# Performance work log

Hardware: AMD Instinct MI355X
Metric: run time of the kernel (lower is better)

The kernel has to match this reference:

```python
import jax, jax.numpy as jnp
import numpy as np

H = 8
D = 512
DK = D // H
B = 16
N = 8192


def setup_inputs() -> dict:
    key = jax.random.key(0)
    k1, k2, k3, k4 = jax.random.split(key, 4)
    x = jax.random.normal(k1, (B, N, D), dtype=jnp.float32)
    W_k = jax.random.normal(k2, (D, D), dtype=jnp.float32) * (1.0 / np.sqrt(D))
    W_g = jax.random.normal(k3, (D, D), dtype=jnp.float32) * (1.0 / np.sqrt(D))
    query = jax.random.normal(k4, (H, 1, DK), dtype=jnp.float32)
    return {"x": x, "W_k": W_k, "W_g": W_g, "query": query}


def reference(x, W_k, W_g, query):
    b, n, d = x.shape
    # nn.Linear: y = x @ W.T  (no bias)
    K = (x @ W_k.T).reshape(b, n, H, DK).transpose(0, 2, 1, 3)  # (b,h,n,dk)
    G = (x @ W_g.T).reshape(b, n, H, DK).transpose(0, 2, 1, 3)  # (b,h,n,dk)
    xh = x.reshape(b, n, H, DK).transpose(0, 2, 1, 3)           # (b,h,n,dk)
    gated = jnp.tanh(K) * jax.nn.sigmoid(G)                     # (b,h,n,dk)
    # single-query attention: scores (b,h,1,n)
    scores = jnp.einsum('hmd,bhnd->bhmn', query, gated)
    attn = jax.nn.softmax(scores, axis=-1)
    out = jnp.einsum('bhmn,bhnd->bhmd', attn, xh)               # (b,h,1,dk)
    out = out.transpose(0, 2, 1, 3).reshape(b, 1, H * DK)
    return out.squeeze()  # (b, d)
```

## Files before the change

kernel.cpp:

```cpp
#include <hip/hip_runtime.h>
#include <hip/hip_bf16.h>

#define H_ 8
#define D_ 512
#define DK_ 64
#define B_ 16
#define N_ 8192
#define M_ (B_ * N_)

typedef __attribute__((ext_vector_type(8))) short short8;
typedef __attribute__((ext_vector_type(4))) float floatx4;

__device__ __forceinline__ void glds16(const void* g, void* l) {
    __builtin_amdgcn_global_load_lds((const __attribute__((address_space(1))) void*)g,
                                     (__attribute__((address_space(3))) void*)l,
                                     16, 0, 0);
}

__device__ __forceinline__ unsigned short f2bf(float f) {
    unsigned u = __float_as_uint(f);
    return (unsigned short)((u + 0x7fffu + ((u >> 16) & 1u)) >> 16);
}

__device__ __forceinline__ unsigned pack_bf2(float x, float y) {
    return __builtin_amdgcn_perm(__float_as_uint(y) + 0x8000u,
                                 __float_as_uint(x) + 0x8000u, 0x07060302u);
}

__global__ __launch_bounds__(256) void cvt_kernel(const float* __restrict__ src,
                                                  unsigned short* __restrict__ dst, int n4) {
    int i = blockIdx.x * blockDim.x + threadIdx.x;
    int stride = gridDim.x * blockDim.x;
    for (; i < n4; i += stride) {
        float4 v = ((const float4*)src)[i];
        ushort4 o;
        o.x = f2bf(v.x); o.y = f2bf(v.y); o.z = f2bf(v.z); o.w = f2bf(v.w);
        ((ushort4*)dst)[i] = o;
    }
}

__global__ __launch_bounds__(256, 2) void gemm_score_kernel(
    const float* __restrict__ x,
    const unsigned short* __restrict__ wkb,
    const unsigned short* __restrict__ wgb,
    const float* __restrict__ query,
    float* __restrict__ s_buf)
{
    __shared__ float lds_a[128 * 32];
    __shared__ unsigned short lds_k[128 * 32];
    __shared__ unsigned short lds_g[128 * 32];

    const int t = threadIdx.x;
    const int lane = t & 63;
    const int wave = t >> 6;
    const int wm = wave >> 1, wn = wave & 1;
    const int jc = blockIdx.x * 128;
    const int m0 = blockIdx.y * 128;

    floatx4 acc_k[4][4], acc_g[4][4];
#pragma unroll
    for (int i = 0; i < 4; ++i)
#pragma unroll
        for (int j = 0; j < 4; ++j) { acc_k[i][j] = (floatx4)0.f; acc_g[i][j] = (floatx4)0.f; }

    int ar[4], ac[4];
#pragma unroll
    for (int i = 0; i < 4; ++i) {
        int p = i * 256 + t;
        int r = p >> 3;
        ar[i] = r;
        ac[i] = (p & 7) ^ (r & 7);
    }
    int br[2], bc[2];
#pragma unroll
    for (int i = 0; i < 2; ++i) {
        int p = i * 256 + t;
        int r = p >> 2;
        br[i] = r;
        bc[i] = (p & 3) ^ ((r >> 1) & 3);
    }

    const int fr = lane & 15;
    const int q  = lane >> 4;
    const int sw_a0 = (2 * q) ^ (fr & 7);
    const int sw_a1 = sw_a0 ^ 1;
    const int sw_b  = q ^ ((fr >> 1) & 3);

    for (int k0 = 0; k0 < 512; k0 += 32) {
#pragma unroll
        for (int i = 0; i < 4; ++i)
            glds16(x + (size_t)(m0 + ar[i]) * 512 + k0 + ac[i] * 4,
                   lds_a + (size_t)(i * 256 + t) * 4);
#pragma unroll
        for (int i = 0; i < 2; ++i) {
            glds16(wkb + (size_t)(jc + br[i]) * 512 + k0 + bc[i] * 8,
                   lds_k + (size_t)(i * 256 + t) * 8);
            glds16(wgb + (size_t)(jc + br[i]) * 512 + k0 + bc[i] * 8,
                   lds_g + (size_t)(i * 256 + t) * 8);
        }
        __syncthreads();

        short8 a[4], bk[4], bg[4];
#pragma unroll
        for (int mi = 0; mi < 4; ++mi) {
            int r = wm * 64 + mi * 16 + fr;
            float4 f0 = *(const float4*)(lds_a + (r * 8 + sw_a0) * 4);
            float4 f1 = *(const float4*)(lds_a + (r * 8 + sw_a1) * 4);
            union { unsigned u[4]; short8 s; } tmp;
            tmp.u[0] = pack_bf2(f0.x, f0.y);
            tmp.u[1] = pack_bf2(f0.z, f0.w);
            tmp.u[2] = pack_bf2(f1.x, f1.y);
            tmp.u[3] = pack_bf2(f1.z, f1.w);
            a[mi] = tmp.s;
        }
#pragma unroll
        for (int ni = 0; ni < 4; ++ni) {
            int r = wn * 64 + ni * 16 + fr;
            bk[ni] = *(const short8*)(lds_k + (r * 4 + sw_b) * 8);
            bg[ni] = *(const short8*)(lds_g + (r * 4 + sw_b) * 8);
        }
#pragma unroll
        for (int mi = 0; mi < 4; ++mi)
#pragma unroll
            for (int ni = 0; ni < 4; ++ni) {
                acc_k[mi][ni] = __builtin_amdgcn_mfma_f32_16x16x32_bf16(a[mi], bk[ni], acc_k[mi][ni], 0, 0, 0);
                acc_g[mi][ni] = __builtin_amdgcn_mfma_f32_16x16x32_bf16(a[mi], bg[ni], acc_g[mi][ni], 0, 0, 0);
            }
        __syncthreads();
    }

    const int h = blockIdx.x * 2 + wn;
    float qv[4];
#pragma unroll
    for (int ni = 0; ni < 4; ++ni) qv[ni] = query[h * 64 + ni * 16 + fr];

#pragma unroll
    for (int mi = 0; mi < 4; ++mi) {
#pragma unroll
        for (int r = 0; r < 4; ++r) {
            float v = 0.f;
#pragma unroll
            for (int ni = 0; ni < 4; ++ni) {
                float kv = acc_k[mi][ni][r];
                float gv = acc_g[mi][ni][r];
                float e2k = __expf(2.f * kv);
                float th = 1.f - 2.f / (e2k + 1.f);
                float sg = 1.f / (1.f + __expf(-gv));
                v += qv[ni] * th * sg;
            }
            v += __shfl_xor(v, 1);
            v += __shfl_xor(v, 2);
            v += __shfl_xor(v, 4);
            v += __shfl_xor(v, 8);
            if (fr == 0) {
                int mg = m0 + wm * 64 + mi * 16 + (lane >> 4) * 4 + r;
                int b = mg >> 13, n = mg & 8191;
                s_buf[((size_t)(b * 8 + h) << 13) + n] = v;
            }
        }
    }
}

__global__ __launch_bounds__(256) void stats_kernel(const float* __restrict__ s_buf,
                                                    float* __restrict__ mb, float* __restrict__ lb) {
    const int bh = blockIdx.x;
    const float* s = s_buf + ((size_t)bh << 13);
    const int t = threadIdx.x;
    float mx = -3.0e38f;
    for (int i = t; i < 8192; i += 256) mx = fmaxf(mx, s[i]);
#pragma unroll
    for (int m = 32; m > 0; m >>= 1) mx = fmaxf(mx, __shfl_xor(mx, m));
    __shared__ float red[8];
    if ((t & 63) == 0) red[t >> 6] = mx;
    __syncthreads();
    mx = fmaxf(fmaxf(red[0], red[1]), fmaxf(red[2], red[3]));
    float sum = 0.f;
    for (int i = t; i < 8192; i += 256) sum += __expf(s[i] - mx);
#pragma unroll
    for (int m = 32; m > 0; m >>= 1) sum += __shfl_xor(sum, m);
    if ((t & 63) == 0) red[4 + (t >> 6)] = sum;
    __syncthreads();
    if (t == 0) { mb[bh] = mx; lb[bh] = red[4] + red[5] + red[6] + red[7]; }
}

__global__ __launch_bounds__(256) void out_kernel(
    const float* __restrict__ x, const float* __restrict__ s_buf,
    const float* __restrict__ mb, const float* __restrict__ lb,
    float* __restrict__ out) {
    const int b = blockIdx.x >> 5;
    const int chunk = blockIdx.x & 31;
    const int n0 = chunk * 256;
    const int t = threadIdx.x;
    __shared__ float w[8 * 256];
    for (int i = t; i < 2048; i += 256) {
        int hh = i >> 8, nn = i & 255;
        int bh = b * 8 + hh;
        w[i] = __expf(s_buf[((size_t)bh << 13) + n0 + nn] - mb[bh]) / lb[bh];
    }
    __syncthreads();
    const int rg = t >> 6;
    const int d0 = (t & 63) * 8;
    const float* wh = w + ((d0 >> 6) << 8);
    float acc[8] = {0.f, 0.f, 0.f, 0.f, 0.f, 0.f, 0.f, 0.f};
    for (int nn = rg; nn < 256; nn += 4) {
        const float4* row = (const float4*)(x + (((size_t)(b * 8192 + n0 + nn)) << 9) + d0);
        float4 v0 = row[0];
        float4 v1 = row[1];
        float ww = wh[nn];
        acc[0] += ww * v0.x; acc[1] += ww * v0.y;
        acc[2] += ww * v0.z; acc[3] += ww * v0.w;
        acc[4] += ww * v1.x; acc[5] += ww * v1.y;
        acc[6] += ww * v1.z; acc[7] += ww * v1.w;
    }
#pragma unroll
    for (int j = 0; j < 8; ++j) atomicAdd(&out[b * 512 + d0 + j], acc[j]);
}

extern "C" void kernel_launch(void* const* d_in, const int* in_sizes, int n_in,
                              void* d_out, int out_size, void* d_ws, size_t ws_size,
                              hipStream_t stream) {
    const float* x  = (const float*)d_in[0];
    const float* Wk = (const float*)d_in[1];
    const float* Wg = (const float*)d_in[2];
    const float* q  = (const float*)d_in[3];
    float* out = (float*)d_out;

    char* ws = (char*)d_ws;
    unsigned short* wkb = (unsigned short*)ws;
    unsigned short* wgb = (unsigned short*)(ws + 524288ull);
    float* s_buf = (float*)(ws + 1048576ull);
    float* mb = (float*)(ws + 5242880ull);
    float* lb = (float*)(ws + 5243392ull);

    hipMemsetAsync(d_out, 0, 512 * B_ * sizeof(float), stream);

    hipLaunchKernelGGL(cvt_kernel, dim3(256), dim3(256), 0, stream, Wk, wkb, (D_ * D_) / 4);
    hipLaunchKernelGGL(cvt_kernel, dim3(256), dim3(256), 0, stream, Wg, wgb, (D_ * D_) / 4);
    hipLaunchKernelGGL(gemm_score_kernel, dim3(4, 1024), dim3(256), 0, stream, x, wkb, wgb, q, s_buf);
    hipLaunchKernelGGL(stats_kernel, dim3(128), dim3(256), 0, stream, s_buf, mb, lb);
    hipLaunchKernelGGL(out_kernel, dim3(512), dim3(256), 0, stream, x, s_buf, mb, lb, out);
}
```

Measured before the change: 630.7 us.

## Convert A tile to bf16 at load, double K-step, remap grid for XCD locality

Loads x through registers and converts it to bf16 once when storing into LDS. Before, fp32 tiles were staged with direct global-to-LDS loads and each wave packed them to bf16 after reading LDS. The K step grows from 32 to 64, halving the number of barrier pairs, and the A tile now takes half the LDS per element. The grid becomes 1D with a remap so that the four column tiles sharing an M tile land on the same XCD, which should improve L2 reuse of x. The cost is that A loads now go through VGPRs, which adds register pressure and loses the asynchronous global-to-LDS path.

```diff
diff --git a/kernel.cpp b/kernel.cpp
--- a/kernel.cpp
+++ b/kernel.cpp
@@ -25,6 +25,15 @@
 __device__ __forceinline__ unsigned pack_bf2(float x, float y) {
     return __builtin_amdgcn_perm(__float_as_uint(y) + 0x8000u,
                                  __float_as_uint(x) + 0x8000u, 0x07060302u);
+}
+
+__device__ __forceinline__ short8 pack_bf8(float4 lo, float4 hi) {
+    union { unsigned u[4]; short8 s; } tmp;
+    tmp.u[0] = pack_bf2(lo.x, lo.y);
+    tmp.u[1] = pack_bf2(lo.z, lo.w);
+    tmp.u[2] = pack_bf2(hi.x, hi.y);
+    tmp.u[3] = pack_bf2(hi.z, hi.w);
+    return tmp.s;
 }
 
 __global__ __launch_bounds__(256) void cvt_kernel(const float* __restrict__ src,
@@ -46,16 +55,22 @@
     const float* __restrict__ query,
     float* __restrict__ s_buf)
 {
-    __shared__ float lds_a[128 * 32];
-    __shared__ unsigned short lds_k[128 * 32];
-    __shared__ unsigned short lds_g[128 * 32];
+    __shared__ unsigned short lds_a[128 * 64];
+    __shared__ unsigned short lds_k[128 * 64];
+    __shared__ unsigned short lds_g[128 * 64];
 
     const int t = threadIdx.x;
     const int lane = t & 63;
     const int wave = t >> 6;
     const int wm = wave >> 1, wn = wave & 1;
-    const int jc = blockIdx.x * 128;
-    const int m0 = blockIdx.y * 128;
+
+    const int g = blockIdx.x;
+    const int xcd = g & 7;
+    const int s = g >> 3;
+    const int jt = s & 3;
+    const int mt = ((s >> 2) << 3) | xcd;
+    const int jc = jt * 128;
+    const int m0 = mt * 128;
 
     floatx4 acc_k[4][4], acc_g[4][4];
 #pragma unroll
@@ -63,73 +78,73 @@
 #pragma unroll
         for (int j = 0; j < 4; ++j) { acc_k[i][j] = (floatx4)0.f; acc_g[i][j] = (floatx4)0.f; }
 
-    int ar[4], ac[4];
+    const int r0 = t >> 2;
+    const int c0 = t & 3;
+    const int swr = ((r0 & 1) << 2) ^ ((r0 >> 1) & 3);
+    const float* pA0 = x + (size_t)(m0 + r0) * 512 + c0 * 8;
+    const float* pA1 = pA0 + 64 * 512;
+    unsigned short* wA00 = lds_a + ((r0 * 8) + (c0 ^ swr)) * 8;
+    unsigned short* wA01 = lds_a + ((r0 * 8) + ((c0 ^ swr) ^ 4)) * 8;
+    unsigned short* wA10 = wA00 + 64 * 64;
+    unsigned short* wA11 = wA01 + 64 * 64;
+
+    int boff[4];
 #pragma unroll
     for (int i = 0; i < 4; ++i) {
         int p = i * 256 + t;
         int r = p >> 3;
-        ar[i] = r;
-        ac[i] = (p & 7) ^ (r & 7);
-    }
-    int br[2], bc[2];
-#pragma unroll
-    for (int i = 0; i < 2; ++i) {
-        int p = i * 256 + t;
-        int r = p >> 2;
-        br[i] = r;
-        bc[i] = (p & 3) ^ ((r >> 1) & 3);
+        int c = (p & 7) ^ (((r & 1) << 2) ^ ((r >> 1) & 3));
+        boff[i] = (jc + r) * 512 + c * 8;
     }
 
     const int fr = lane & 15;
     const int q  = lane >> 4;
-    const int sw_a0 = (2 * q) ^ (fr & 7);
-    const int sw_a1 = sw_a0 ^ 1;
-    const int sw_b  = q ^ ((fr >> 1) & 3);
-
-    for (int k0 = 0; k0 < 512; k0 += 32) {
-#pragma unroll
-        for (int i = 0; i < 4; ++i)
-            glds16(x + (size_t)(m0 + ar[i]) * 512 + k0 + ac[i] * 4,
-                   lds_a + (size_t)(i * 256 + t) * 4);
-#pragma unroll
-        for (int i = 0; i < 2; ++i) {
-            glds16(wkb + (size_t)(jc + br[i]) * 512 + k0 + bc[i] * 8,
-                   lds_k + (size_t)(i * 256 + t) * 8);
-            glds16(wgb + (size_t)(jc + br[i]) * 512 + k0 + bc[i] * 8,
-                   lds_g + (size_t)(i * 256 + t) * 8);
+    const int swf = ((fr & 1) << 2) ^ ((fr >> 1) & 3);
+
+    for (int k0 = 0; k0 < 512; k0 += 64) {
+#pragma unroll
+        for (int i = 0; i < 4; ++i) {
+            glds16(wkb + boff[i] + k0, lds_k + (size_t)(i * 256 + t) * 8);
+            glds16(wgb + boff[i] + k0, lds_g + (size_t)(i * 256 + t) * 8);
+        }
+        float4 a00 = *(const float4*)(pA0 + k0);
+        float4 a01 = *(const float4*)(pA0 + k0 + 4);
+        float4 a02 = *(const float4*)(pA0 + k0 + 32);
+        float4 a03 = *(const float4*)(pA0 + k0 + 36);
+        float4 a10 = *(const float4*)(pA1 + k0);
+        float4 a11 = *(const float4*)(pA1 + k0 + 4);
+        float4 a12 = *(const float4*)(pA1 + k0 + 32);
+        float4 a13 = *(const float4*)(pA1 + k0 + 36);
+        *(short8*)wA00 = pack_bf8(a00, a01);
+        *(short8*)wA01 = pack_bf8(a02, a03);
+        *(short8*)wA10 = pack_bf8(a10, a11);
+        *(short8*)wA11 = pack_bf8(a12, a13);
+        __syncthreads();
+
+#pragma unroll
+        for (int kc = 0; kc < 2; ++kc) {
+            const int sl = ((kc * 4 + q) ^ swf) * 8;
+            short8 a[4], bk[4], bg[4];
+#pragma unroll
+            for (int mi = 0; mi < 4; ++mi)
+                a[mi] = *(const short8*)(lds_a + (wm * 64 + mi * 16 + fr) * 64 + sl);
+#pragma unroll
+            for (int ni = 0; ni < 4; ++ni) {
+                bk[ni] = *(const short8*)(lds_k + (wn * 64 + ni * 16 + fr) * 64 + sl);
+                bg[ni] = *(const short8*)(lds_g + (wn * 64 + ni * 16 + fr) * 64 + sl);
+            }
+#pragma unroll
+            for (int mi = 0; mi < 4; ++mi)
+#pragma unroll
+                for (int ni = 0; ni < 4; ++ni) {
+                    acc_k[mi][ni] = __builtin_amdgcn_mfma_f32_16x16x32_bf16(a[mi], bk[ni], acc_k[mi][ni], 0, 0, 0);
+                    acc_g[mi][ni] = __builtin_amdgcn_mfma_f32_16x16x32_bf16(a[mi], bg[ni], acc_g[mi][ni], 0, 0, 0);
+                }
         }
         __syncthreads();
-
-        short8 a[4], bk[4], bg[4];
-#pragma unroll
-        for (int mi = 0; mi < 4; ++mi) {
-            int r = wm * 64 + mi * 16 + fr;
-            float4 f0 = *(const float4*)(lds_a + (r * 8 + sw_a0) * 4);
-            float4 f1 = *(const float4*)(lds_a + (r * 8 + sw_a1) * 4);
-            union { unsigned u[4]; short8 s; } tmp;
-            tmp.u[0] = pack_bf2(f0.x, f0.y);
-            tmp.u[1] = pack_bf2(f0.z, f0.w);
-            tmp.u[2] = pack_bf2(f1.x, f1.y);
-            tmp.u[3] = pack_bf2(f1.z, f1.w);
-            a[mi] = tmp.s;
-        }
-#pragma unroll
-        for (int ni = 0; ni < 4; ++ni) {
-            int r = wn * 64 + ni * 16 + fr;
-            bk[ni] = *(const short8*)(lds_k + (r * 4 + sw_b) * 8);
-            bg[ni] = *(const short8*)(lds_g + (r * 4 + sw_b) * 8);
-        }
-#pragma unroll
-        for (int mi = 0; mi < 4; ++mi)
-#pragma unroll
-            for (int ni = 0; ni < 4; ++ni) {
-                acc_k[mi][ni] = __builtin_amdgcn_mfma_f32_16x16x32_bf16(a[mi], bk[ni], acc_k[mi][ni], 0, 0, 0);
-                acc_g[mi][ni] = __builtin_amdgcn_mfma_f32_16x16x32_bf16(a[mi], bg[ni], acc_g[mi][ni], 0, 0, 0);
-            }
-        __syncthreads();
-    }
-
-    const int h = blockIdx.x * 2 + wn;
+    }
+
+    const int h = jt * 2 + wn;
     float qv[4];
 #pragma unroll
     for (int ni = 0; ni < 4; ++ni) qv[ni] = query[h * 64 + ni * 16 + fr];
@@ -236,7 +251,7 @@
 
     hipLaunchKernelGGL(cvt_kernel, dim3(256), dim3(256), 0, stream, Wk, wkb, (D_ * D_) / 4);
     hipLaunchKernelGGL(cvt_kernel, dim3(256), dim3(256), 0, stream, Wg, wgb, (D_ * D_) / 4);
-    hipLaunchKernelGGL(gemm_score_kernel, dim3(4, 1024), dim3(256), 0, stream, x, wkb, wgb, q, s_buf);
+    hipLaunchKernelGGL(gemm_score_kernel, dim3(4096), dim3(256), 0, stream, x, wkb, wgb, q, s_buf);
     hipLaunchKernelGGL(stats_kernel, dim3(128), dim3(256), 0, stream, s_buf, mb, lb);
     hipLaunchKernelGGL(out_kernel, dim3(512), dim3(256), 0, stream, x, s_buf, mb, lb, out);
 }
```

Measured after the change: 584.7 us. 1.08x faster.
